# Kernel tuning notes

Hardware: AMD Instinct MI355X
Metric: run time of the kernel (lower is better)

## Reference

```python
import jax, jax.numpy as jnp
import numpy as np

N, D = 1024, 256


def setup_inputs() -> dict:
    key = jax.random.key(0)
    k1, k2 = jax.random.split(key)
    mu_X = jax.random.normal(k1, (N, D), dtype=jnp.float32)
    log_sigma = jax.random.normal(k2, (N, D), dtype=jnp.float32)
    return {"mu_X": mu_X, "log_sigma": log_sigma}


def reference(mu_X, log_sigma):
    # F.normalize: x / max(||x||_2, eps), eps=1e-12
    norm = jnp.linalg.norm(mu_X, axis=-1, keepdims=True)
    mu = mu_X / jnp.maximum(norm, 1e-12)
    sigma_sq = jnp.exp(log_sigma)                       # [N, D]
    sig_sum = sigma_sq[:, None, :] + sigma_sq[None, :, :]  # [N, N, D]
    # pairwise squared diff weighted by summed variances + log-variance penalty
    diff = (mu[:, None, :] - mu[None, :, :]) ** 2 / (1e-10 + sig_sum) + jnp.log(sig_sum)
    return -diff.sum(axis=2)                            # [N, N]
```

## Files before the change

### kernel.cpp

```cpp
#include <hip/hip_runtime.h>

#define N 1024
#define D 256
#define RI 32

__global__ __launch_bounds__(256) void prep2(
    const float* __restrict__ muX, const float* __restrict__ ls,
    float4* __restrict__ msT4) {
  const int i0 = blockIdx.x * RI;
  const int t = threadIdx.x;
  __shared__ float sred[RI][8];
  __shared__ float rden[RI];
  const int r = t >> 3, q = t & 7;
  const float4* rowp = (const float4*)(muX + (size_t)(i0 + r) * D);
  float s = 0.f;
#pragma unroll
  for (int k = 0; k < 8; ++k) {
    const float4 v = rowp[q + 8 * k];
    s += v.x * v.x + v.y * v.y + v.z * v.z + v.w * v.w;
  }
  sred[r][q] = s;
  __syncthreads();
  if (q == 0) {
    float tot = 0.f;
    for (int u = 0; u < 8; ++u) tot += sred[r][u];
    rden[r] = 1.0f / fmaxf(sqrtf(tot), 1e-12f);
  }
  __syncthreads();
  const int w = t >> 6, l = t & 63;
  const int il = l >> 1, b = l & 1;
  const float rd = rden[il];
  const int row = i0 + il;
  float2* outp = (float2*)msT4;
  for (int it = 0; it < 32; ++it) {
    const int g = it * 4 + w;
    const int d = 2 * g + b;
    const float mu = muX[(size_t)row * D + d] * rd;
    const float sg = __expf(ls[(size_t)row * D + d]) + 5e-11f;
    outp[((size_t)g * N + row) * 2 + b] = make_float2(mu, sg);
  }
}

__global__ __launch_bounds__(128) void pair_kernel(
    const float4* __restrict__ msT4, float* __restrict__ out) {
  int L = blockIdx.x;
  int js = 0, base = 0;
  while (L >= base + 32 * (js + 1)) { base += 32 * (js + 1); ++js; }
  const int ib = L - base;
  const int j0 = js * 128, i0 = ib * 4;
  const bool diag = (ib >= js * 32);
  const int j = j0 + threadIdx.x;

  float acc[4] = {0.f, 0.f, 0.f, 0.f};
  float p[4] = {1.f, 1.f, 1.f, 1.f};
  int ea[4] = {0, 0, 0, 0};

#pragma unroll 4
  for (int g = 0; g < D / 2; ++g) {
    const float4 jv = msT4[(size_t)g * N + j];
#pragma unroll
    for (int k = 0; k < 4; ++k) {
      const float4 iv = msT4[(size_t)g * N + i0 + k];
      {
        const float sv = iv.y + jv.y;
        const float t0 = iv.x - jv.x;
        acc[k] = fmaf(t0 * t0, __builtin_amdgcn_rcpf(sv), acc[k]);
        p[k] *= sv;
      }
      {
        const float sv = iv.w + jv.w;
        const float t0 = iv.z - jv.z;
        acc[k] = fmaf(t0 * t0, __builtin_amdgcn_rcpf(sv), acc[k]);
        p[k] *= sv;
      }
    }
    if (g & 1) {
#pragma unroll
      for (int k = 0; k < 4; ++k) {
        const int bb = __float_as_int(p[k]);
        ea[k] += bb >> 23;
        p[k] = __int_as_float((bb & 0x007fffff) | 0x3f800000);
      }
    }
  }

  constexpr float LN2 = 0.6931471805599453f;
  float v[4];
#pragma unroll
  for (int k = 0; k < 4; ++k) {
    const float lg2 = (float)(ea[k] - 127 * (D / 4)) + __log2f(p[k]);
    v[k] = -(acc[k] + LN2 * lg2);
  }

  if (!diag) {
#pragma unroll
    for (int k = 0; k < 4; ++k) out[(size_t)(i0 + k) * N + j] = v[k];
    float4 m;
    m.x = v[0]; m.y = v[1]; m.z = v[2]; m.w = v[3];
    *(float4*)(out + (size_t)j * N + i0) = m;
  } else {
#pragma unroll
    for (int k = 0; k < 4; ++k) {
      const int i = i0 + k;
      if (j >= i) out[(size_t)i * N + j] = v[k];
      if (j > i) out[(size_t)j * N + i] = v[k];
    }
  }
}

extern "C" void kernel_launch(void* const* d_in, const int* in_sizes, int n_in,
                              void* d_out, int out_size, void* d_ws, size_t ws_size,
                              hipStream_t stream) {
  const float* muX = (const float*)d_in[0];
  const float* ls  = (const float*)d_in[1];
  float* out = (float*)d_out;
  float4* msT4 = (float4*)d_ws;
  prep2<<<dim3(N / RI), dim3(256), 0, stream>>>(muX, ls, msT4);
  pair_kernel<<<dim3(1152), dim3(128), 0, stream>>>(msT4, out);
}
```

Before: 106.9 us.

## Stage prep rows through LDS and software-prefetch pair-kernel loads

The prep kernel now handles 8 rows per block. It loads mu and exp(log_sigma) into shared memory with coalesced float4 reads, reduces the norms there, and then writes the transposed interleaved layout. This gives 128 blocks instead of 32 and avoids strided global reads. The pair kernel double-buffers its register loads, issuing the next two groups' loads before computing the current pair. This is meant to hide global load latency, at the cost of more live registers, with the mantissa renormalisation still done every two groups.

```diff
diff --git a/kernel.cpp b/kernel.cpp
--- a/kernel.cpp
+++ b/kernel.cpp
@@ -2,44 +2,72 @@
 
 #define N 1024
 #define D 256
-#define RI 32
 
-__global__ __launch_bounds__(256) void prep2(
+#define RI 8
+#define LDW 260
+
+__global__ __launch_bounds__(256) void prep3(
     const float* __restrict__ muX, const float* __restrict__ ls,
-    float4* __restrict__ msT4) {
+    float2* __restrict__ msT2) {
   const int i0 = blockIdx.x * RI;
   const int t = threadIdx.x;
-  __shared__ float sred[RI][8];
+  __shared__ float smu[RI][LDW];
+  __shared__ float ssg[RI][LDW];
+  __shared__ float sred[RI][32];
   __shared__ float rden[RI];
-  const int r = t >> 3, q = t & 7;
-  const float4* rowp = (const float4*)(muX + (size_t)(i0 + r) * D);
-  float s = 0.f;
+  const float4* mu4 = (const float4*)(muX + (size_t)i0 * D);
+  const float4* ls4 = (const float4*)(ls + (size_t)i0 * D);
 #pragma unroll
-  for (int k = 0; k < 8; ++k) {
-    const float4 v = rowp[q + 8 * k];
-    s += v.x * v.x + v.y * v.y + v.z * v.z + v.w * v.w;
-  }
-  sred[r][q] = s;
-  __syncthreads();
-  if (q == 0) {
-    float tot = 0.f;
-    for (int u = 0; u < 8; ++u) tot += sred[r][u];
-    rden[r] = 1.0f / fmaxf(sqrtf(tot), 1e-12f);
+  for (int u = 0; u < 2; ++u) {
+    const int idx = u * 256 + t;
+    const int row = idx >> 6, c4 = idx & 63;
+    const float4 v = mu4[idx];
+    *(float4*)&smu[row][c4 * 4] = v;
+    const float4 e = ls4[idx];
+    float4 x;
+    x.x = __expf(e.x) + 5e-11f; x.y = __expf(e.y) + 5e-11f;
+    x.z = __expf(e.z) + 5e-11f; x.w = __expf(e.w) + 5e-11f;
+    *(float4*)&ssg[row][c4 * 4] = x;
   }
   __syncthreads();
-  const int w = t >> 6, l = t & 63;
-  const int il = l >> 1, b = l & 1;
-  const float rd = rden[il];
-  const int row = i0 + il;
-  float2* outp = (float2*)msT4;
-  for (int it = 0; it < 32; ++it) {
-    const int g = it * 4 + w;
+  {
+    const int r = t >> 5, q = t & 31;
+    float s = 0.f;
+#pragma unroll
+    for (int k = 0; k < 8; ++k) {
+      const float v = smu[r][q + 32 * k];
+      s = fmaf(v, v, s);
+    }
+    sred[r][q] = s;
+  }
+  __syncthreads();
+  if (t < RI) {
+    float tot = 0.f;
+    for (int u = 0; u < 32; ++u) tot += sred[t][u];
+    rden[t] = 1.0f / fmaxf(sqrtf(tot), 1e-12f);
+  }
+  __syncthreads();
+#pragma unroll
+  for (int pass = 0; pass < 8; ++pass) {
+    const int f = pass * 256 + t;
+    const int b = f & 1, il = (f >> 1) & 7, g = f >> 4;
     const int d = 2 * g + b;
-    const float mu = muX[(size_t)row * D + d] * rd;
-    const float sg = __expf(ls[(size_t)row * D + d]) + 5e-11f;
-    outp[((size_t)g * N + row) * 2 + b] = make_float2(mu, sg);
+    msT2[((size_t)g * N + i0 + il) * 2 + b] =
+        make_float2(smu[il][d] * rden[il], ssg[il][d]);
   }
 }
+
+#define UPD(jv, iv, k)                                           \
+  {                                                              \
+    const float s0 = (iv).y + (jv).y;                            \
+    const float t0 = (iv).x - (jv).x;                            \
+    acc[k] = fmaf(t0 * t0, __builtin_amdgcn_rcpf(s0), acc[k]);   \
+    p[k] *= s0;                                                  \
+    const float s1 = (iv).w + (jv).w;                            \
+    const float t1 = (iv).z - (jv).z;                            \
+    acc[k] = fmaf(t1 * t1, __builtin_amdgcn_rcpf(s1), acc[k]);   \
+    p[k] *= s1;                                                  \
+  }
 
 __global__ __launch_bounds__(128) void pair_kernel(
     const float4* __restrict__ msT4, float* __restrict__ out) {
@@ -51,37 +79,41 @@
   const bool diag = (ib >= js * 32);
   const int j = j0 + threadIdx.x;
 
+  const float4* __restrict__ pj = msT4 + j;
+  const float4* __restrict__ pi = msT4 + i0;
+
   float acc[4] = {0.f, 0.f, 0.f, 0.f};
   float p[4] = {1.f, 1.f, 1.f, 1.f};
   int ea[4] = {0, 0, 0, 0};
 
-#pragma unroll 4
-  for (int g = 0; g < D / 2; ++g) {
-    const float4 jv = msT4[(size_t)g * N + j];
+  float4 jA = pj[0];
+  float4 jB = pj[(size_t)N];
+  float4 iA0 = pi[0], iA1 = pi[1], iA2 = pi[2], iA3 = pi[3];
+  float4 iB0 = pi[N + 0], iB1 = pi[N + 1], iB2 = pi[N + 2], iB3 = pi[N + 3];
+
+  for (int g = 0; g < D / 2; g += 2) {
+    const size_t o2 = (size_t)((g + 2 < D / 2) ? g + 2 : 0) * N;
+    const size_t o3 = (size_t)((g + 3 < D / 2) ? g + 3 : 0) * N;
+    const float4 njA = pj[o2];
+    const float4 niA0 = pi[o2 + 0], niA1 = pi[o2 + 1];
+    const float4 niA2 = pi[o2 + 2], niA3 = pi[o2 + 3];
+    const float4 njB = pj[o3];
+    const float4 niB0 = pi[o3 + 0], niB1 = pi[o3 + 1];
+    const float4 niB2 = pi[o3 + 2], niB3 = pi[o3 + 3];
+
+    UPD(jA, iA0, 0) UPD(jA, iA1, 1) UPD(jA, iA2, 2) UPD(jA, iA3, 3)
+    UPD(jB, iB0, 0) UPD(jB, iB1, 1) UPD(jB, iB2, 2) UPD(jB, iB3, 3)
+
 #pragma unroll
     for (int k = 0; k < 4; ++k) {
-      const float4 iv = msT4[(size_t)g * N + i0 + k];
-      {
-        const float sv = iv.y + jv.y;
-        const float t0 = iv.x - jv.x;
-        acc[k] = fmaf(t0 * t0, __builtin_amdgcn_rcpf(sv), acc[k]);
-        p[k] *= sv;
-      }
-      {
-        const float sv = iv.w + jv.w;
-        const float t0 = iv.z - jv.z;
-        acc[k] = fmaf(t0 * t0, __builtin_amdgcn_rcpf(sv), acc[k]);
-        p[k] *= sv;
-      }
+      const int bb = __float_as_int(p[k]);
+      ea[k] += bb >> 23;
+      p[k] = __int_as_float((bb & 0x007fffff) | 0x3f800000);
     }
-    if (g & 1) {
-#pragma unroll
-      for (int k = 0; k < 4; ++k) {
-        const int bb = __float_as_int(p[k]);
-        ea[k] += bb >> 23;
-        p[k] = __int_as_float((bb & 0x007fffff) | 0x3f800000);
-      }
-    }
+
+    jA = njA; jB = njB;
+    iA0 = niA0; iA1 = niA1; iA2 = niA2; iA3 = niA3;
+    iB0 = niB0; iB1 = niB1; iB2 = niB2; iB3 = niB3;
   }
 
   constexpr float LN2 = 0.6931471805599453f;
@@ -114,7 +146,8 @@
   const float* muX = (const float*)d_in[0];
   const float* ls  = (const float*)d_in[1];
   float* out = (float*)d_out;
-  float4* msT4 = (float4*)d_ws;
-  prep2<<<dim3(N / RI), dim3(256), 0, stream>>>(muX, ls, msT4);
-  pair_kernel<<<dim3(1152), dim3(128), 0, stream>>>(msT4, out);
+  float2* msT2 = (float2*)d_ws;
+  prep3<<<dim3(N / RI), dim3(256), 0, stream>>>(muX, ls, msT2);
+  pair_kernel<<<dim3(1152), dim3(128), 0, stream>>>((const float4*)msT2,
+                                                    out);
 }
```

Result: faster. 100.1 us (-6.4%).
